# Kernel tuning notes

Measured on AMD Instinct MI355X. Metric: run time of the kernel, lower is better.

Reference implementation:

```python
import jax, jax.numpy as jnp
import numpy as np

B, N, C, H = 8, 1024, 512, 8
EPS = 1e-6


def setup_inputs() -> dict:
    key = jax.random.key(0)
    k0, k1, k2, k3, k4 = jax.random.split(key, 5)
    x = jax.random.normal(k0, (B, N, C), dtype=jnp.float32)
    # nonnegative random-walk visit-frequency mask stand-in
    mask = jax.random.uniform(k1, (N, N), dtype=jnp.float32)
    w_qkv = jax.random.normal(k2, (C, 3 * C), dtype=jnp.float32) * 0.02
    w_out = jax.random.normal(k3, (C, C), dtype=jnp.float32) * 0.02
    b_out = jax.random.normal(k4, (C,), dtype=jnp.float32) * 0.02
    return {"x": x, "mask": mask, "w_qkv": w_qkv, "w_out": w_out, "b_out": b_out}


def reference(x, mask, w_qkv, w_out, b_out):
    b, n, c = x.shape
    d = c // H
    qkv = x @ w_qkv                                   # [B,N,3C]
    q, k, v = jnp.split(qkv, 3, axis=-1)

    def to_heads(t):
        return t.reshape(b, n, H, d).transpose(0, 2, 1, 3)  # [B,H,N,D]

    q, k, v = to_heads(q), to_heads(k), to_heads(v)
    # positive feature map
    q = jax.nn.relu(q) + EPS
    k = jax.nn.relu(k) + EPS
    # graph diffusion: (q^T @ mask)^T == einsum over source node m
    q = q + 0.1 * jnp.einsum('bhmd,mn->bhnd', q, mask)
    k = k + 0.1 * jnp.einsum('bhmd,mn->bhnd', k, mask)
    # linear kernel scores, elementwise-masked
    kernel = jnp.einsum('bhnd,bhmd->bhnm', q, k) * mask   # [B,H,N,N]
    z = 1.0 / (kernel.sum(axis=-1, keepdims=True) + EPS)  # [B,H,N,1]
    out = jnp.einsum('bhnm,bhmd->bhnd', kernel, v) * z    # [B,H,N,D]
    out = out.transpose(0, 2, 1, 3).reshape(b, n, c)      # [B,N,C]
    return out @ w_out + b_out
```

## Files before the change

kernel.cpp:

```cpp
#include <hip/hip_runtime.h>
#include <cstddef>

#define Bsz 8
#define Nn  1024
#define Cc  512
#define Hh  8
#define Dd  64
#define EPSF 1e-6f

typedef __attribute__((ext_vector_type(8))) short short8;
typedef __attribute__((ext_vector_type(4))) float floatx4;

static __device__ __forceinline__ short f2bf(float f) {
    union { float f; unsigned u; } v; v.f = f;
    unsigned r = (v.u + 0x7FFFu + ((v.u >> 16) & 1u)) >> 16;
    return (short)r;
}
static __device__ __forceinline__ float bf2f(short s) {
    union { unsigned u; float f; } v; v.u = ((unsigned)(unsigned short)s) << 16;
    return v.f;
}

#define GLOAD_LDS16(gp, lp)                                              \
    __builtin_amdgcn_global_load_lds(                                    \
        (const __attribute__((address_space(1))) void*)(gp),             \
        (__attribute__((address_space(3))) void*)(lp), 16, 0, 0)

static __device__ __forceinline__
void stage_tile(short* __restrict__ lds, const short* __restrict__ src,
                int ldsrc, int tid, int CHUNKS, int SLOTS) {
    #pragma unroll
    for (int s = tid; s < SLOTS; s += 256) {
        int r = s / CHUNKS, cs = s % CHUNKS;
        int gc = cs ^ (r & 7);
        GLOAD_LDS16(&src[(size_t)r * ldsrc + gc * 8], &lds[s * 8]);
    }
}
static __device__ __forceinline__
short8 fragT(const short* __restrict__ lds, int CHUNKS, int r, int lc) {
    return *(const short8*)&lds[(r * CHUNKS + (lc ^ (r & 7))) * 8];
}

#define FENCE() asm volatile("" ::: "memory")
#define BARRIER_RAW() do { FENCE(); __builtin_amdgcn_s_barrier(); FENCE(); } while (0)
#define WAITVM(N) asm volatile("s_waitcnt vmcnt(" #N ")" ::: "memory")

__global__ __launch_bounds__(256)
void prep_all(const float* __restrict__ x, const float* __restrict__ mask,
              const float* __restrict__ wq, const float* __restrict__ wo,
              short* __restrict__ xb, short* __restrict__ Ad,
              short* __restrict__ wqT, short* __restrict__ woT,
              short* __restrict__ mbf) {
    __shared__ float t[64][65];
    const int tid = threadIdx.x;
    const int bid = blockIdx.x;

    if (bid < 2048) {
        int idx = bid * 256 + tid;
        const float* s = &x[(size_t)idx * 8];
        union { short h[8]; int4 v; } u;
        #pragma unroll
        for (int j = 0; j < 8; j++) u.h[j] = f2bf(s[j]);
        *(int4*)&xb[(size_t)idx * 8] = u.v;
        return;
    }
    if (bid < 2304) {
        int idx = bid - 2048;
        const int n0 = (idx & 15) * 64, m0 = (idx >> 4) * 64;
        #pragma unroll
        for (int i = 0; i < 4; i++) {
            int k = i * 256 + tid;
            int r = k >> 4, c4 = (k & 15) * 4;
            *(float4*)&t[r][c4] = *(const float4*)&mask[(size_t)(m0 + r) * Nn + n0 + c4];
        }
        __syncthreads();
        #pragma unroll
        for (int i = 0; i < 4; i++) {
            int k = i * 256 + tid;
            int rr = k >> 4, c4 = (k & 15) * 4;
            union { short h[4]; int2 v; } u;
            #pragma unroll
            for (int j = 0; j < 4; j++) {
                int mm = c4 + j;
                float v = 0.1f * t[mm][rr] + ((n0 + rr) == (m0 + mm) ? 1.0f : 0.0f);
                u.h[j] = f2bf(v);
            }
            *(int2*)&Ad[(size_t)(n0 + rr) * Nn + m0 + c4] = u.v;
        }
        return;
    }
    if (bid < 2496) {
        int idx = bid - 2304;
        const int n0 = (idx % 24) * 64, k0 = (idx / 24) * 64;
        #pragma unroll
        for (int i = 0; i < 4; i++) {
            int k = i * 256 + tid;
            int r = k >> 4, c4 = (k & 15) * 4;
            *(float4*)&t[r][c4] = *(const float4*)&wq[(size_t)(k0 + r) * 1536 + n0 + c4];
        }
        __syncthreads();
        #pragma unroll
        for (int i = 0; i < 4; i++) {
            int k = i * 256 + tid;
            int rr = k >> 4, c4 = (k & 15) * 4;
            union { short h[4]; int2 v; } u;
            #pragma unroll
            for (int j = 0; j < 4; j++) u.h[j] = f2bf(t[c4 + j][rr]);
            *(int2*)&wqT[(size_t)(n0 + rr) * 512 + k0 + c4] = u.v;
        }
        return;
    }
    if (bid < 2560) {
        int idx = bid - 2496;
        const int n0 = (idx & 7) * 64, k0 = (idx >> 3) * 64;
        #pragma unroll
        for (int i = 0; i < 4; i++) {
            int k = i * 256 + tid;
            int r = k >> 4, c4 = (k & 15) * 4;
            *(float4*)&t[r][c4] = *(const float4*)&wo[(size_t)(k0 + r) * 512 + n0 + c4];
        }
        __syncthreads();
        #pragma unroll
        for (int i = 0; i < 4; i++) {
            int k = i * 256 + tid;
            int rr = k >> 4, c4 = (k & 15) * 4;
            union { short h[4]; int2 v; } u;
            #pragma unroll
            for (int j = 0; j < 4; j++) u.h[j] = f2bf(t[c4 + j][rr]);
            *(int2*)&woT[(size_t)(n0 + rr) * 512 + k0 + c4] = u.v;
        }
        return;
    }
    {
        int idx = (bid - 2560) * 256 + tid;
        const float* s = &mask[(size_t)idx * 8];
        union { short h[8]; int4 v; } u;
        #pragma unroll
        for (int j = 0; j < 8; j++) u.h[j] = f2bf(s[j]);
        *(int4*)&mbf[(size_t)idx * 8] = u.v;
    }
}

static __device__ __forceinline__
void stageA_half(short* __restrict__ buf, const short* __restrict__ gA,
                 int kt, int h, int tid) {
    #pragma unroll
    for (int kk = 0; kk < 2; kk++) {
        int i = tid + kk * 512;
        int run = i >> 9;
        int within = i & 511;
        int r = run * 128 + h * 64 + (within >> 3);
        int c = within & 7;
        int gc = c ^ (r & 7);
        GLOAD_LDS16(gA + (size_t)r * 512 + kt + gc * 8, buf + (r * 8 + c) * 8);
    }
}
static __device__ __forceinline__
void stageB_half(short* __restrict__ buf, const short* __restrict__ gB,
                 int kt, int h, int tid) {
    #pragma unroll
    for (int kk = 0; kk < 2; kk++) {
        int i = tid + kk * 512;
        int run = i >> 8;
        int within = i & 255;
        int r = run * 64 + h * 32 + (within >> 3);
        int c = within & 7;
        int gc = c ^ (r & 7);
        GLOAD_LDS16(gB + (size_t)r * 512 + kt + gc * 8, buf + (r * 8 + c) * 8);
    }
}

template<int MH>
static __device__ __forceinline__
void readA8(const short* __restrict__ bufA, short8 (&aF)[4][2],
            int wr, int l16, int quad) {
    #pragma unroll
    for (int f = 0; f < 4; f++)
        #pragma unroll
        for (int kk = 0; kk < 2; kk++)
            aF[f][kk] = fragT(bufA, 8, wr * 128 + MH * 64 + f * 16 + l16, kk * 4 + quad);
}
template<int NH>
static __device__ __forceinline__
void readB4(const short* __restrict__ bufB, short8 (&bF)[2][2],
            int wc, int l16, int quad) {
    #pragma unroll
    for (int g = 0; g < 2; g++)
        #pragma unroll
        for (int kk = 0; kk < 2; kk++)
            bF[g][kk] = fragT(bufB, 8, wc * 64 + NH * 32 + g * 16 + l16, kk * 4 + quad);
}
template<int MH, int NH>
static __device__ __forceinline__
void mfma16(short8 (&aF)[4][2], short8 (&bF)[2][2], floatx4 (&acc)[8][4]) {
    #pragma unroll
    for (int kk = 0; kk < 2; kk++)
        #pragma unroll
        for (int f = 0; f < 4; f++)
            #pragma unroll
            for (int g = 0; g < 2; g++)
                acc[MH * 4 + f][NH * 2 + g] = __builtin_amdgcn_mfma_f32_16x16x32_bf16(
                    aF[f][kk], bF[g][kk], acc[MH * 4 + f][NH * 2 + g], 0, 0, 0);
}

__global__ __launch_bounds__(512, 2)
void gemm_qkv(const short* __restrict__ xb, const short* __restrict__ wqT,
              short* __restrict__ qT, short* __restrict__ kT,
              short* __restrict__ vT) {
    extern __shared__ short smem[];

    const int tid = threadIdx.x;
    const int lin = blockIdx.x;
    const int wgid = (lin & 7) * 24 + (lin >> 3);
    const int mt = wgid / 6, nt = wgid % 6;
    const int m0 = mt * 256, n0 = nt * 256;

    const int wid = tid >> 6, lane = tid & 63;
    const int quad = lane >> 4, l16 = lane & 15;
    const int wr = wid >> 2, wc = wid & 3;

    const short* Ab = xb  + (size_t)m0 * 512;
    const short* Bb = wqT + (size_t)n0 * 512;

    floatx4 acc[8][4];
    #pragma unroll
    for (int i = 0; i < 8; i++)
        #pragma unroll
        for (int j = 0; j < 4; j++) acc[i][j] = (floatx4){0.f, 0.f, 0.f, 0.f};

    short8 aF[4][2], bF[2][2];

    stageA_half(smem,          Ab, 0, 0, tid);
    stageB_half(smem + 16384,  Bb, 0, 0, tid);
    stageA_half(smem,          Ab, 0, 1, tid);
    stageB_half(smem + 16384,  Bb, 0, 1, tid);
    WAITVM(4); BARRIER_RAW();

    for (int j = 0; j < 8; ++j) {
        const short* cA = smem + (j & 1) * 32768;
        const short* cB = cA + 16384;
        short* nA = smem + ((j + 1) & 1) * 32768;
        short* nB = nA + 16384;
        const int kn = ((j + 1) & 7) * 64;

        readA8<0>(cA, aF, wr, l16, quad);
        readB4<0>(cB, bF, wc, l16, quad);
        stageA_half(nA, Ab, kn, 0, tid);
        stageB_half(nB, Bb, kn, 0, tid);
        BARRIER_RAW();
        __builtin_amdgcn_s_setprio(1);
        mfma16<0, 0>(aF, bF, acc);
        __builtin_amdgcn_s_setprio(0);
        WAITVM(4); BARRIER_RAW();

        readA8<1>(cA, aF, wr, l16, quad);
        stageA_half(nA, Ab, kn, 1, tid);
        stageB_half(nB, Bb, kn, 1, tid);
        BARRIER_RAW();
        __builtin_amdgcn_s_setprio(1);
        mfma16<1, 0>(aF, bF, acc);
        __builtin_amdgcn_s_setprio(0);
        BARRIER_RAW();

        readB4<1>(cB, bF, wc, l16, quad);
        BARRIER_RAW();
        __builtin_amdgcn_s_setprio(1);
        mfma16<1, 1>(aF, bF, acc);
        __builtin_amdgcn_s_setprio(0);
        BARRIER_RAW();

        readA8<0>(cA, aF, wr, l16, quad);
        BARRIER_RAW();
        __builtin_amdgcn_s_setprio(1);
        mfma16<0, 1>(aF, bF, acc);
        __builtin_amdgcn_s_setprio(0);
        WAITVM(4); BARRIER_RAW();
    }

    WAITVM(0); BARRIER_RAW();

    short* T = smem + wid * 8192;
    const int doRelu = (n0 < 1024);
    #pragma unroll
    for (int mf = 0; mf < 8; mf++)
        #pragma unroll
        for (int nf = 0; nf < 4; nf++)
            #pragma unroll
            for (int rr = 0; rr < 4; rr++) {
                float v = acc[mf][nf][rr];
                if (doRelu) v = fmaxf(v, 0.0f) + EPSF;
                int row = nf * 16 + l16;
                int col = mf * 16 + quad * 4 + rr;
                T[row * 128 + (col ^ ((row & 15) << 3))] = f2bf(v);
            }
    const int gm0 = m0 + wr * 128;
    const int b = gm0 >> 10, m_in0 = gm0 & 1023;
    #pragma unroll
    for (int g = 0; g < 4; g++) {
        int row = (lane >> 2) + g * 16;
        int gn = n0 + wc * 64 + row;
        int part = gn >> 9, ci = gn & 511;
        short* base = (part == 0) ? qT : (part == 1) ? kT : vT;
        short* dst = base + ((size_t)b * 512 + ci) * 1024 + m_in0;
        #pragma unroll
        for (int cc = 0; cc < 4; cc++) {
            int cs = ((lane & 3) + cc * 4) * 8;
            *(int4*)&dst[cs] = *(const int4*)&T[row * 128 + (cs ^ ((row & 15) << 3))];
        }
    }
}

static __device__ __forceinline__
void dstageA_half(short* __restrict__ buf, const short* __restrict__ gA,
                  int kt, int h, int tid) {
    #pragma unroll
    for (int kk = 0; kk < 2; kk++) {
        int i = tid + kk * 512;
        int rl = i >> 3;
        int c  = i & 7;
        int r  = (rl >> 5) * 64 + h * 32 + (rl & 31);
        int gc = c ^ (r & 7);
        GLOAD_LDS16(gA + (size_t)r * 1024 + kt + gc * 8, buf + (r * 8 + c) * 8);
    }
}
static __device__ __forceinline__
void dstageB_half(short* __restrict__ buf, const short* __restrict__ gB,
                  int kt, int h, int tid) {
    int rl = tid >> 3;
    int c  = tid & 7;
    int r  = (rl >> 5) * 64 + h * 32 + (rl & 31);
    int gc = c ^ (r & 7);
    GLOAD_LDS16(gB + (size_t)r * 1024 + kt + gc * 8, buf + (r * 8 + c) * 8);
}
template<int MH>
static __device__ __forceinline__
void dreadA(const short* __restrict__ bufA, short8 (&aF)[2][2],
            int wr, int l16, int quad) {
    #pragma unroll
    for (int f = 0; f < 2; f++)
        #pragma unroll
        for (int kk = 0; kk < 2; kk++)
            aF[f][kk] = fragT(bufA, 8, wr * 64 + MH * 32 + f * 16 + l16, kk * 4 + quad);
}
template<int NH>
static __device__ __forceinline__
void dreadB(const short* __restrict__ bufB, short8 (&bF)[2][2],
            int wc, int l16, int quad) {
    #pragma unroll
    for (int g = 0; g < 2; g++)
        #pragma unroll
        for (int kk = 0; kk < 2; kk++)
            bF[g][kk] = fragT(bufB, 8, wc * 64 + NH * 32 + g * 16 + l16, kk * 4 + quad);
}
template<int MH, int NH>
static __device__ __forceinline__
void dmfma8(short8 (&aF)[2][2], short8 (&bF)[2][2], floatx4 (&acc)[4][4]) {
    #pragma unroll
    for (int kk = 0; kk < 2; kk++)
        #pragma unroll
        for (int f = 0; f < 2; f++)
            #pragma unroll
            for (int g = 0; g < 2; g++)
                acc[MH * 2 + f][NH * 2 + g] = __builtin_amdgcn_mfma_f32_16x16x32_bf16(
                    aF[f][kk], bF[g][kk], acc[MH * 2 + f][NH * 2 + g], 0, 0, 0);
}

__global__ __launch_bounds__(512, 2)
void gemm_diff8(const short* __restrict__ Ad, const short* __restrict__ qT,
                const short* __restrict__ kT, short* __restrict__ qd,
                short* __restrict__ kd) {
    extern __shared__ short smem[];

    const int tid = threadIdx.x;
    const int lin = blockIdx.x;
    const int wgid = (lin & 7) * 32 + (lin >> 3);
    const int mt = wgid >> 6, ct = wgid & 63;
    const int m0 = mt * 256;
    const int seg = ct >> 2, cb = (ct & 3) * 128;
    const int b = seg >> 1, part = seg & 1;

    const short* Bb = ((part ? kT : qT) + (size_t)b * 512 * 1024) + (size_t)cb * 1024;
    short* outb = (part ? kd : qd) + (size_t)b * 1024 * 512;
    const short* Abase = Ad + (size_t)m0 * 1024;

    const int wid = tid >> 6, lane = tid & 63;
    const int quad = lane >> 4, l16 = lane & 15;
    const int wr = wid >> 1, wc = wid & 1;

    floatx4 acc[4][4];
    #pragma unroll
    for (int i = 0; i < 4; i++)
        #pragma unroll
        for (int j = 0; j < 4; j++) acc[i][j] = (floatx4){0.f, 0.f, 0.f, 0.f};

    short8 aF[2][2], bF[2][2];

    dstageA_half(smem,          Abase, 0, 0, tid);
    dstageB_half(smem + 16384,  Bb,    0, 0, tid);
    dstageA_half(smem,          Abase, 0, 1, tid);
    dstageB_half(smem + 16384,  Bb,    0, 1, tid);
    WAITVM(3); BARRIER_RAW();

    for (int j = 0; j < 16; ++j) {
        const short* cA = smem + (j & 1) * 24576;
        const short* cB = cA + 16384;
        short* nA = smem + ((j + 1) & 1) * 24576;
        short* nB = nA + 16384;
        const int kn = ((j + 1) & 15) * 64;

        dreadA<0>(cA, aF, wr, l16, quad);
        dreadB<0>(cB, bF, wc, l16, quad);
        dstageA_half(nA, Abase, kn, 0, tid);
        dstageB_half(nB, Bb,    kn, 0, tid);
        BARRIER_RAW();
        __builtin_amdgcn_s_setprio(1);
        dmfma8<0, 0>(aF, bF, acc);
        __builtin_amdgcn_s_setprio(0);
        WAITVM(3); BARRIER_RAW();

        dreadA<1>(cA, aF, wr, l16, quad);
        dstageA_half(nA, Abase, kn, 1, tid);
        dstageB_half(nB, Bb,    kn, 1, tid);
        BARRIER_RAW();
        __builtin_amdgcn_s_setprio(1);
        dmfma8<1, 0>(aF, bF, acc);
        __builtin_amdgcn_s_setprio(0);
        BARRIER_RAW();

        dreadB<1>(cB, bF, wc, l16, quad);
        BARRIER_RAW();
        __builtin_amdgcn_s_setprio(1);
        dmfma8<1, 1>(aF, bF, acc);
        __builtin_amdgcn_s_setprio(0);
        BARRIER_RAW();

        dreadA<0>(cA, aF, wr, l16, quad);
        BARRIER_RAW();
        __builtin_amdgcn_s_setprio(1);
        dmfma8<0, 1>(aF, bF, acc);
        __builtin_amdgcn_s_setprio(0);
        WAITVM(3); BARRIER_RAW();
    }
    WAITVM(0);

    #pragma unroll
    for (int fr = 0; fr < 4; fr++)
        #pragma unroll
        for (int rr = 0; rr < 4; rr++) {
            int n = m0 + wr * 64 + fr * 16 + quad * 4 + rr;
            #pragma unroll
            for (int fc = 0; fc < 4; fc++) {
                int c = cb + wc * 64 + fc * 16 + l16;
                outb[(size_t)n * 512 + c] = f2bf(acc[fr][fc][rr]);
            }
        }
}

__global__ __launch_bounds__(256)
void attn_mfma(const short* __restrict__ qd, const short* __restrict__ kd,
               const short* __restrict__ vTg, const short* __restrict__ mbf,
               short* __restrict__ abf) {
    __shared__ short qs[8192];
    __shared__ short ks[4096];
    __shared__ short vt[4096];
    __shared__ short ss[8192];
    __shared__ short ms[8192];

    const int tid = threadIdx.x;
    const int bh = blockIdx.x;
    const int b = bh >> 3, h = bh & 7;
    const int n0 = blockIdx.y * 128;

    const int wave = tid >> 6, lane = tid & 63;
    const int quad = lane >> 4, l16 = lane & 15;

    const short* Qb = qd + ((size_t)b * Nn + n0) * Cc + h * Dd;
    const short* Kb = kd + (size_t)b * Nn * Cc + h * Dd;
    const short* Vb = vTg + ((size_t)b * Cc + h * Dd) * Nn;
    const short* Mb = mbf + (size_t)n0 * Nn;

    stage_tile(qs, Qb, Cc, tid, 8, 1024);
    __syncthreads();
    short8 aT[2][2];
    #pragma unroll
    for (int t = 0; t < 2; t++) {
        aT[t][0] = fragT(qs, 8, wave * 32 + t * 16 + l16, quad);
        aT[t][1] = fragT(qs, 8, wave * 32 + t * 16 + l16, 4 + quad);
    }

    float dreg[2] = {0.f, 0.f};
    floatx4 nacc[2][4];
    #pragma unroll
    for (int t = 0; t < 2; t++)
        #pragma unroll
        for (int i = 0; i < 4; i++) nacc[t][i] = (floatx4){0.f, 0.f, 0.f, 0.f};

    const int ssrow[2] = { wave * 32 + l16, wave * 32 + 16 + l16 };

    for (int m0 = 0; m0 < Nn; m0 += 64) {
        __syncthreads();
        stage_tile(ks, Kb + (size_t)m0 * Cc, Cc, tid, 8, 512);
        stage_tile(vt, Vb + m0, Nn, tid, 8, 512);
        stage_tile(ms, Mb + m0, Nn, tid, 8, 1024);
        __syncthreads();

        #pragma unroll
        for (int mt = 0; mt < 4; mt++) {
            const short8 k0f = fragT(ks, 8, mt * 16 + l16, quad);
            const short8 k1f = fragT(ks, 8, mt * 16 + l16, 4 + quad);
            #pragma unroll
            for (int t = 0; t < 2; t++) {
                floatx4 s = (floatx4){0.f, 0.f, 0.f, 0.f};
                s = __builtin_amdgcn_mfma_f32_16x16x32_bf16(k0f, aT[t][0], s, 0, 0, 0);
                s = __builtin_amdgcn_mfma_f32_16x16x32_bf16(k1f, aT[t][1], s, 0, 0, 0);
                const int row = ssrow[t];
                const int c = mt * 16 + quad * 4;
                const int off = (row * 8 + ((c >> 3) ^ (row & 7))) * 8 + (c & 7);
                union { short h[4]; int2 v; } mk;
                mk.v = *(const int2*)&ms[off];
                float sv0 = s[0] * bf2f(mk.h[0]);
                float sv1 = s[1] * bf2f(mk.h[1]);
                float sv2 = s[2] * bf2f(mk.h[2]);
                float sv3 = s[3] * bf2f(mk.h[3]);
                dreg[t] += (sv0 + sv1) + (sv2 + sv3);
                union { short h[4]; int2 v; } pk;
                pk.h[0] = f2bf(sv0); pk.h[1] = f2bf(sv1);
                pk.h[2] = f2bf(sv2); pk.h[3] = f2bf(sv3);
                *(int2*)&ss[off] = pk.v;
            }
        }

        short8 p[2][2];
        #pragma unroll
        for (int t = 0; t < 2; t++) {
            p[t][0] = fragT(ss, 8, wave * 32 + t * 16 + l16, quad);
            p[t][1] = fragT(ss, 8, wave * 32 + t * 16 + l16, 4 + quad);
        }
        #pragma unroll
        for (int dt = 0; dt < 4; dt++) {
            const short8 v0 = fragT(vt, 8, dt * 16 + l16, quad);
            const short8 v1 = fragT(vt, 8, dt * 16 + l16, 4 + quad);
            #pragma unroll
            for (int t = 0; t < 2; t++) {
                nacc[t][dt] = __builtin_amdgcn_mfma_f32_16x16x32_bf16(p[t][0], v0, nacc[t][dt], 0, 0, 0);
                nacc[t][dt] = __builtin_amdgcn_mfma_f32_16x16x32_bf16(p[t][1], v1, nacc[t][dt], 0, 0, 0);
            }
        }
    }

    #pragma unroll
    for (int t = 0; t < 2; t++) {
        dreg[t] += __shfl_xor(dreg[t], 16, 64);
        dreg[t] += __shfl_xor(dreg[t], 32, 64);
    }

    #pragma unroll
    for (int t = 0; t < 2; t++)
        #pragma unroll
        for (int r = 0; r < 4; r++) {
            int nloc = quad * 4 + r;
            float den = __shfl(dreg[t], nloc, 64);
            int n = n0 + wave * 32 + t * 16 + nloc;
            float zr = 1.0f / (den + EPSF);
            #pragma unroll
            for (int dt = 0; dt < 4; dt++) {
                size_t o = ((size_t)b * Nn + n) * Cc + h * Dd + dt * 16 + l16;
                abf[o] = f2bf(nacc[t][dt][r] * zr);
            }
        }
}

__global__ __launch_bounds__(256)
void gemm_out(const short* __restrict__ abf, const short* __restrict__ woT,
              const float* __restrict__ bias, float* __restrict__ out) {
    __shared__ short smem[12288];
    short* As = smem;
    short* Bs = smem + 4096;

    const int tid = threadIdx.x;
    const int m0 = blockIdx.y * 64;
    const int n0 = blockIdx.x * 128;
    const int wave = tid >> 6, lane = tid & 63;
    const int quad = lane >> 4, l16 = lane & 15;
    const int wm = (wave >> 1) * 32, wn = (wave & 1) * 64;

    floatx4 acc[2][4];
    #pragma unroll
    for (int i = 0; i < 2; i++)
        #pragma unroll
        for (int j = 0; j < 4; j++) acc[i][j] = (floatx4){0.f, 0.f, 0.f, 0.f};

    const short* Ab = abf + (size_t)m0 * 512;
    const short* Bb = woT + (size_t)n0 * 512;

    for (int k0 = 0; k0 < 512; k0 += 64) {
        __syncthreads();
        stage_tile(As, Ab + k0, 512, tid, 8, 512);
        stage_tile(Bs, Bb + k0, 512, tid, 8, 1024);
        __syncthreads();
        #pragma unroll
        for (int kh = 0; kh < 2; kh++) {
            short8 a[2], b[4];
            #pragma unroll
            for (int i = 0; i < 2; i++)
                a[i] = fragT(As, 8, wm + i * 16 + l16, kh * 4 + quad);
            #pragma unroll
            for (int i = 0; i < 4; i++)
                b[i] = fragT(Bs, 8, wn + i * 16 + l16, kh * 4 + quad);
            #pragma unroll
            for (int mi = 0; mi < 2; mi++)
                #pragma unroll
                for (int ni = 0; ni < 4; ni++)
                    acc[mi][ni] = __builtin_amdgcn_mfma_f32_16x16x32_bf16(
                        a[mi], b[ni], acc[mi][ni], 0, 0, 0);
        }
    }

    #pragma unroll
    for (int mi = 0; mi < 2; mi++)
        #pragma unroll
        for (int r = 0; r < 4; r++) {
            int m = m0 + wm + mi * 16 + quad * 4 + r;
            #pragma unroll
            for (int ni = 0; ni < 4; ni++) {
                int n = n0 + wn + ni * 16 + l16;
                out[(size_t)m * 512 + n] = acc[mi][ni][r] + bias[n];
            }
        }
}

extern "C" void kernel_launch(void* const* d_in, const int* in_sizes, int n_in,
                              void* d_out, int out_size, void* d_ws, size_t ws_size,
                              hipStream_t stream) {
    const float* x     = (const float*)d_in[0];
    const float* mask  = (const float*)d_in[1];
    const float* w_qkv = (const float*)d_in[2];
    const float* w_out = (const float*)d_in[3];
    const float* b_out = (const float*)d_in[4];
    float* out = (float*)d_out;

    char* p = (char*)d_ws;
    short* xb  = (short*)p; p += 8388608;
    short* wqT = (short*)p; p += 1572864;
    short* Ad  = (short*)p; p += 2097152;
    short* woT = (short*)p; p += 524288;
    short* mbf = (short*)p; p += 2097152;
    short* qT  = (short*)p; p += 8388608;
    short* kT  = (short*)p; p += 8388608;
    short* vT  = (short*)p; p += 8388608;
    short* qd  = (short*)p; p += 8388608;
    short* kd  = (short*)p; p += 8388608;
    short* abf = (short*)p; p += 8388608;

    static int attr_set = 0;
    if (!attr_set) {
        hipFuncSetAttribute(reinterpret_cast<const void*>(gemm_qkv),
                            hipFuncAttributeMaxDynamicSharedMemorySize, 131072);
        hipFuncSetAttribute(reinterpret_cast<const void*>(gemm_diff8),
                            hipFuncAttributeMaxDynamicSharedMemorySize, 98304);
        attr_set = 1;
    }

    dim3 blk(256);

    prep_all  <<<3072, blk, 0, stream>>>(x, mask, w_qkv, w_out,
                                         xb, Ad, wqT, woT, mbf);
    gemm_qkv  <<<dim3(192), dim3(512), 131072, stream>>>(xb, wqT, qT, kT, vT);
    gemm_diff8<<<dim3(256), dim3(512), 98304, stream>>>(Ad, qT, kT, qd, kd);
    attn_mfma <<<dim3(64, 8),  blk, 0, stream>>>(qd, kd, vT, mbf, abf);
    gemm_out  <<<dim3(4, 128), blk, 0, stream>>>(abf, woT, b_out, out);
}
```

Baseline: 166.2 us.

## Double-buffer K/V tiles in attention kernel and load mask directly to registers

Restructures the attention kernel's main loop into a two-stage ping-pong pipeline. The next K/V tile is staged into a second LDS buffer while the current tile is computed. Mask values are loaded straight from global memory into registers instead of going through LDS, and the Q staging buffer is reused for the score scratch once Q fragments are in registers. It also packs bf16 conversion with v_cvt_pk_bf16_f32 and raises wave priority around the PV MFMAs. The goal is to hide global load latency and cut barriers and LDS traffic, at the cost of more registers and reliance on raw barrier and waitcnt ordering for correctness.

```diff
diff --git a/kernel.cpp b/kernel.cpp
--- a/kernel.cpp
+++ b/kernel.cpp
@@ -456,15 +456,63 @@
         }
 }
 
+static __device__ __forceinline__
+void attn_tile(const short* __restrict__ ks, const short* __restrict__ vt,
+               short* __restrict__ ss, const int2 (&M)[2][4],
+               const short8 (&aT)[2][2], float (&dreg)[2],
+               floatx4 (&nacc)[2][4], int wave, int quad, int l16) {
+    const int ssrow[2] = { wave * 32 + l16, wave * 32 + 16 + l16 };
+    #pragma unroll
+    for (int mt = 0; mt < 4; mt++) {
+        const short8 k0f = fragT(ks, 8, mt * 16 + l16, quad);
+        const short8 k1f = fragT(ks, 8, mt * 16 + l16, 4 + quad);
+        #pragma unroll
+        for (int t = 0; t < 2; t++) {
+            floatx4 s = (floatx4){0.f, 0.f, 0.f, 0.f};
+            s = __builtin_amdgcn_mfma_f32_16x16x32_bf16(k0f, aT[t][0], s, 0, 0, 0);
+            s = __builtin_amdgcn_mfma_f32_16x16x32_bf16(k1f, aT[t][1], s, 0, 0, 0);
+            const int row = ssrow[t];
+            const int c = mt * 16 + quad * 4;
+            const int off = (row * 8 + ((c >> 3) ^ (row & 7))) * 8 + (c & 7);
+            union { short hh[4]; int2 v; } mk; mk.v = M[t][mt];
+            float sv0 = s[0] * bf2f(mk.hh[0]);
+            float sv1 = s[1] * bf2f(mk.hh[1]);
+            float sv2 = s[2] * bf2f(mk.hh[2]);
+            float sv3 = s[3] * bf2f(mk.hh[3]);
+            dreg[t] += (sv0 + sv1) + (sv2 + sv3);
+            int lo, hi;
+            asm("v_cvt_pk_bf16_f32 %0, %1, %2" : "=v"(lo) : "v"(sv0), "v"(sv1));
+            asm("v_cvt_pk_bf16_f32 %0, %1, %2" : "=v"(hi) : "v"(sv2), "v"(sv3));
+            int2 pv; pv.x = lo; pv.y = hi;
+            *(int2*)&ss[off] = pv;
+        }
+    }
+    short8 p[2][2];
+    #pragma unroll
+    for (int t = 0; t < 2; t++) {
+        p[t][0] = fragT(ss, 8, wave * 32 + t * 16 + l16, quad);
+        p[t][1] = fragT(ss, 8, wave * 32 + t * 16 + l16, 4 + quad);
+    }
+    __builtin_amdgcn_s_setprio(1);
+    #pragma unroll
+    for (int dt = 0; dt < 4; dt++) {
+        const short8 v0 = fragT(vt, 8, dt * 16 + l16, quad);
+        const short8 v1 = fragT(vt, 8, dt * 16 + l16, 4 + quad);
+        #pragma unroll
+        for (int t = 0; t < 2; t++) {
+            nacc[t][dt] = __builtin_amdgcn_mfma_f32_16x16x32_bf16(p[t][0], v0, nacc[t][dt], 0, 0, 0);
+            nacc[t][dt] = __builtin_amdgcn_mfma_f32_16x16x32_bf16(p[t][1], v1, nacc[t][dt], 0, 0, 0);
+        }
+    }
+    __builtin_amdgcn_s_setprio(0);
+}
+
 __global__ __launch_bounds__(256)
 void attn_mfma(const short* __restrict__ qd, const short* __restrict__ kd,
                const short* __restrict__ vTg, const short* __restrict__ mbf,
                short* __restrict__ abf) {
-    __shared__ short qs[8192];
-    __shared__ short ks[4096];
-    __shared__ short vt[4096];
-    __shared__ short ss[8192];
-    __shared__ short ms[8192];
+    __shared__ short qss[8192];
+    __shared__ short kv[2][8192];
 
     const int tid = threadIdx.x;
     const int bh = blockIdx.x;
@@ -477,15 +525,24 @@
     const short* Qb = qd + ((size_t)b * Nn + n0) * Cc + h * Dd;
     const short* Kb = kd + (size_t)b * Nn * Cc + h * Dd;
     const short* Vb = vTg + ((size_t)b * Cc + h * Dd) * Nn;
-    const short* Mb = mbf + (size_t)n0 * Nn;
-
-    stage_tile(qs, Qb, Cc, tid, 8, 1024);
-    __syncthreads();
+    const short* baseM = mbf + (size_t)(n0 + wave * 32 + l16) * Nn + quad * 4;
+
+    stage_tile(qss, Qb, Cc, tid, 8, 1024);
+    stage_tile(kv[0],        Kb, Cc, tid, 8, 512);
+    stage_tile(kv[0] + 4096, Vb, Nn, tid, 8, 512);
+    int2 Ma[2][4], Mb2[2][4];
+    #pragma unroll
+    for (int t = 0; t < 2; t++)
+        #pragma unroll
+        for (int mt = 0; mt < 4; mt++)
+            Ma[t][mt] = *(const int2*)(baseM + t * 16 * Nn + mt * 16);
+    WAITVM(0); BARRIER_RAW();
+
     short8 aT[2][2];
     #pragma unroll
     for (int t = 0; t < 2; t++) {
-        aT[t][0] = fragT(qs, 8, wave * 32 + t * 16 + l16, quad);
-        aT[t][1] = fragT(qs, 8, wave * 32 + t * 16 + l16, 4 + quad);
+        aT[t][0] = fragT(qss, 8, wave * 32 + t * 16 + l16, quad);
+        aT[t][1] = fragT(qss, 8, wave * 32 + t * 16 + l16, 4 + quad);
     }
 
     float dreg[2] = {0.f, 0.f};
@@ -495,57 +552,29 @@
         #pragma unroll
         for (int i = 0; i < 4; i++) nacc[t][i] = (floatx4){0.f, 0.f, 0.f, 0.f};
 
-    const int ssrow[2] = { wave * 32 + l16, wave * 32 + 16 + l16 };
-
-    for (int m0 = 0; m0 < Nn; m0 += 64) {
-        __syncthreads();
-        stage_tile(ks, Kb + (size_t)m0 * Cc, Cc, tid, 8, 512);
-        stage_tile(vt, Vb + m0, Nn, tid, 8, 512);
-        stage_tile(ms, Mb + m0, Nn, tid, 8, 1024);
-        __syncthreads();
-
-        #pragma unroll
-        for (int mt = 0; mt < 4; mt++) {
-            const short8 k0f = fragT(ks, 8, mt * 16 + l16, quad);
-            const short8 k1f = fragT(ks, 8, mt * 16 + l16, 4 + quad);
-            #pragma unroll
-            for (int t = 0; t < 2; t++) {
-                floatx4 s = (floatx4){0.f, 0.f, 0.f, 0.f};
-                s = __builtin_amdgcn_mfma_f32_16x16x32_bf16(k0f, aT[t][0], s, 0, 0, 0);
-                s = __builtin_amdgcn_mfma_f32_16x16x32_bf16(k1f, aT[t][1], s, 0, 0, 0);
-                const int row = ssrow[t];
-                const int c = mt * 16 + quad * 4;
-                const int off = (row * 8 + ((c >> 3) ^ (row & 7))) * 8 + (c & 7);
-                union { short h[4]; int2 v; } mk;
-                mk.v = *(const int2*)&ms[off];
-                float sv0 = s[0] * bf2f(mk.h[0]);
-                float sv1 = s[1] * bf2f(mk.h[1]);
-                float sv2 = s[2] * bf2f(mk.h[2]);
-                float sv3 = s[3] * bf2f(mk.h[3]);
-                dreg[t] += (sv0 + sv1) + (sv2 + sv3);
-                union { short h[4]; int2 v; } pk;
-                pk.h[0] = f2bf(sv0); pk.h[1] = f2bf(sv1);
-                pk.h[2] = f2bf(sv2); pk.h[3] = f2bf(sv3);
-                *(int2*)&ss[off] = pk.v;
-            }
-        }
-
-        short8 p[2][2];
-        #pragma unroll
-        for (int t = 0; t < 2; t++) {
-            p[t][0] = fragT(ss, 8, wave * 32 + t * 16 + l16, quad);
-            p[t][1] = fragT(ss, 8, wave * 32 + t * 16 + l16, 4 + quad);
-        }
-        #pragma unroll
-        for (int dt = 0; dt < 4; dt++) {
-            const short8 v0 = fragT(vt, 8, dt * 16 + l16, quad);
-            const short8 v1 = fragT(vt, 8, dt * 16 + l16, 4 + quad);
-            #pragma unroll
-            for (int t = 0; t < 2; t++) {
-                nacc[t][dt] = __builtin_amdgcn_mfma_f32_16x16x32_bf16(p[t][0], v0, nacc[t][dt], 0, 0, 0);
-                nacc[t][dt] = __builtin_amdgcn_mfma_f32_16x16x32_bf16(p[t][1], v1, nacc[t][dt], 0, 0, 0);
-            }
-        }
+    for (int jo = 0; jo < 8; jo++) {
+        const int j0 = jo * 2;
+        stage_tile(kv[1],        Kb + (size_t)(j0 + 1) * 64 * Cc, Cc, tid, 8, 512);
+        stage_tile(kv[1] + 4096, Vb + (j0 + 1) * 64,              Nn, tid, 8, 512);
+        #pragma unroll
+        for (int t = 0; t < 2; t++)
+            #pragma unroll
+            for (int mt = 0; mt < 4; mt++)
+                Mb2[t][mt] = *(const int2*)(baseM + t * 16 * Nn + (j0 + 1) * 64 + mt * 16);
+        attn_tile(kv[0], kv[0] + 4096, qss, Ma, aT, dreg, nacc, wave, quad, l16);
+        WAITVM(0); BARRIER_RAW();
+
+        if (jo < 7) {
+            stage_tile(kv[0],        Kb + (size_t)(j0 + 2) * 64 * Cc, Cc, tid, 8, 512);
+            stage_tile(kv[0] + 4096, Vb + (j0 + 2) * 64,              Nn, tid, 8, 512);
+            #pragma unroll
+            for (int t = 0; t < 2; t++)
+                #pragma unroll
+                for (int mt = 0; mt < 4; mt++)
+                    Ma[t][mt] = *(const int2*)(baseM + t * 16 * Nn + (j0 + 2) * 64 + mt * 16);
+        }
+        attn_tile(kv[1], kv[1] + 4096, qss, Mb2, aT, dreg, nacc, wave, quad, l16);
+        WAITVM(0); BARRIER_RAW();
     }
 
     #pragma unroll
```

Measured after the change: 174.4 us. +5.0%, slower.

## Use 32x32x16 MFMA in attention and keep scores in registers via lane shuffles

Applied to the files above, without the earlier changes.

Rewrites the attention inner loop around 32x32x16 bf16 MFMA instead of 16x16x32. The masked score tile goes straight from the S accumulator layout into the A-operand layout of the PV MFMA through packed bf16 conversions and cross-half lane shuffles, which removes the shared-memory round trip through ss. It also raises wave priority around the PV MFMAs. The aims are fewer LDS writes and reads, less shared memory per block, and better MFMA efficiency. The cost is more shuffle and select instructions and a fragile register layout mapping.

```diff
diff --git a/kernel.cpp b/kernel.cpp
--- a/kernel.cpp
+++ b/kernel.cpp
@@ -10,6 +10,7 @@
 
 typedef __attribute__((ext_vector_type(8))) short short8;
 typedef __attribute__((ext_vector_type(4))) float floatx4;
+typedef __attribute__((ext_vector_type(16))) float floatx16;
 
 static __device__ __forceinline__ short f2bf(float f) {
     union { float f; unsigned u; } v; v.f = f;
@@ -463,7 +464,6 @@
     __shared__ short qs[8192];
     __shared__ short ks[4096];
     __shared__ short vt[4096];
-    __shared__ short ss[8192];
     __shared__ short ms[8192];
 
     const int tid = threadIdx.x;
@@ -472,7 +472,7 @@
     const int n0 = blockIdx.y * 128;
 
     const int wave = tid >> 6, lane = tid & 63;
-    const int quad = lane >> 4, l16 = lane & 15;
+    const int l32 = lane & 31, hi = lane >> 5;
 
     const short* Qb = qd + ((size_t)b * Nn + n0) * Cc + h * Dd;
     const short* Kb = kd + (size_t)b * Nn * Cc + h * Dd;
@@ -481,21 +481,15 @@
 
     stage_tile(qs, Qb, Cc, tid, 8, 1024);
     __syncthreads();
-    short8 aT[2][2];
-    #pragma unroll
-    for (int t = 0; t < 2; t++) {
-        aT[t][0] = fragT(qs, 8, wave * 32 + t * 16 + l16, quad);
-        aT[t][1] = fragT(qs, 8, wave * 32 + t * 16 + l16, 4 + quad);
-    }
-
-    float dreg[2] = {0.f, 0.f};
-    floatx4 nacc[2][4];
-    #pragma unroll
-    for (int t = 0; t < 2; t++)
-        #pragma unroll
-        for (int i = 0; i < 4; i++) nacc[t][i] = (floatx4){0.f, 0.f, 0.f, 0.f};
-
-    const int ssrow[2] = { wave * 32 + l16, wave * 32 + 16 + l16 };
+    short8 qf[4];
+    #pragma unroll
+    for (int j = 0; j < 4; j++)
+        qf[j] = fragT(qs, 8, wave * 32 + l32, 2 * j + hi);
+
+    float dreg = 0.f;
+    floatx16 nacc0, nacc1;
+    #pragma unroll
+    for (int i = 0; i < 16; i++) { nacc0[i] = 0.f; nacc1[i] = 0.f; }
 
     for (int m0 = 0; m0 < Nn; m0 += 64) {
         __syncthreads();
@@ -505,68 +499,83 @@
         __syncthreads();
 
         #pragma unroll
-        for (int mt = 0; mt < 4; mt++) {
-            const short8 k0f = fragT(ks, 8, mt * 16 + l16, quad);
-            const short8 k1f = fragT(ks, 8, mt * 16 + l16, 4 + quad);
-            #pragma unroll
-            for (int t = 0; t < 2; t++) {
-                floatx4 s = (floatx4){0.f, 0.f, 0.f, 0.f};
-                s = __builtin_amdgcn_mfma_f32_16x16x32_bf16(k0f, aT[t][0], s, 0, 0, 0);
-                s = __builtin_amdgcn_mfma_f32_16x16x32_bf16(k1f, aT[t][1], s, 0, 0, 0);
-                const int row = ssrow[t];
-                const int c = mt * 16 + quad * 4;
-                const int off = (row * 8 + ((c >> 3) ^ (row & 7))) * 8 + (c & 7);
-                union { short h[4]; int2 v; } mk;
+        for (int msub = 0; msub < 2; msub++) {
+            floatx16 S;
+            #pragma unroll
+            for (int i = 0; i < 16; i++) S[i] = 0.f;
+            #pragma unroll
+            for (int j = 0; j < 4; j++) {
+                const short8 kf = fragT(ks, 8, msub * 32 + l32, 2 * j + hi);
+                S = __builtin_amdgcn_mfma_f32_32x32x16_bf16(kf, qf[j], S, 0, 0, 0);
+            }
+            const int mrow = wave * 32 + l32;
+            float sv[16];
+            int w[8];
+            #pragma unroll
+            for (int g = 0; g < 4; g++) {
+                const int c = msub * 4 + g;
+                const int off = (mrow * 8 + (c ^ (mrow & 7))) * 8 + hi * 4;
+                union { short hh[4]; int2 v; } mk;
                 mk.v = *(const int2*)&ms[off];
-                float sv0 = s[0] * bf2f(mk.h[0]);
-                float sv1 = s[1] * bf2f(mk.h[1]);
-                float sv2 = s[2] * bf2f(mk.h[2]);
-                float sv3 = s[3] * bf2f(mk.h[3]);
-                dreg[t] += (sv0 + sv1) + (sv2 + sv3);
-                union { short h[4]; int2 v; } pk;
-                pk.h[0] = f2bf(sv0); pk.h[1] = f2bf(sv1);
-                pk.h[2] = f2bf(sv2); pk.h[3] = f2bf(sv3);
-                *(int2*)&ss[off] = pk.v;
+                #pragma unroll
+                for (int ri = 0; ri < 4; ri++) {
+                    float s = S[4 * g + ri] * bf2f(mk.hh[ri]);
+                    sv[4 * g + ri] = s;
+                    dreg += s;
+                }
+                int wl, wh;
+                asm("v_cvt_pk_bf16_f32 %0, %1, %2"
+                    : "=v"(wl) : "v"(sv[4 * g]), "v"(sv[4 * g + 1]));
+                asm("v_cvt_pk_bf16_f32 %0, %1, %2"
+                    : "=v"(wh) : "v"(sv[4 * g + 2]), "v"(sv[4 * g + 3]));
+                w[2 * g] = wl; w[2 * g + 1] = wh;
             }
-        }
-
-        short8 p[2][2];
-        #pragma unroll
-        for (int t = 0; t < 2; t++) {
-            p[t][0] = fragT(ss, 8, wave * 32 + t * 16 + l16, quad);
-            p[t][1] = fragT(ss, 8, wave * 32 + t * 16 + l16, 4 + quad);
-        }
-        #pragma unroll
-        for (int dt = 0; dt < 4; dt++) {
-            const short8 v0 = fragT(vt, 8, dt * 16 + l16, quad);
-            const short8 v1 = fragT(vt, 8, dt * 16 + l16, 4 + quad);
-            #pragma unroll
-            for (int t = 0; t < 2; t++) {
-                nacc[t][dt] = __builtin_amdgcn_mfma_f32_16x16x32_bf16(p[t][0], v0, nacc[t][dt], 0, 0, 0);
-                nacc[t][dt] = __builtin_amdgcn_mfma_f32_16x16x32_bf16(p[t][1], v1, nacc[t][dt], 0, 0, 0);
+            int sx[8];
+            #pragma unroll
+            for (int i = 0; i < 8; i++) sx[i] = __shfl_xor(w[i], 32, 64);
+            union { int wi[4]; short8 v; } pa0, pa1;
+            pa0.wi[0] = hi ? sx[2] : w[0];
+            pa0.wi[1] = hi ? sx[3] : w[1];
+            pa0.wi[2] = hi ? w[2]  : sx[0];
+            pa0.wi[3] = hi ? w[3]  : sx[1];
+            pa1.wi[0] = hi ? sx[6] : w[4];
+            pa1.wi[1] = hi ? sx[7] : w[5];
+            pa1.wi[2] = hi ? w[6]  : sx[4];
+            pa1.wi[3] = hi ? w[7]  : sx[5];
+            __builtin_amdgcn_s_setprio(1);
+            {
+                const short8 v00 = fragT(vt, 8, 0 * 32 + l32, msub * 4 + 0 + hi);
+                const short8 v01 = fragT(vt, 8, 0 * 32 + l32, msub * 4 + 2 + hi);
+                nacc0 = __builtin_amdgcn_mfma_f32_32x32x16_bf16(pa0.v, v00, nacc0, 0, 0, 0);
+                nacc0 = __builtin_amdgcn_mfma_f32_32x32x16_bf16(pa1.v, v01, nacc0, 0, 0, 0);
+                const short8 v10 = fragT(vt, 8, 1 * 32 + l32, msub * 4 + 0 + hi);
+                const short8 v11 = fragT(vt, 8, 1 * 32 + l32, msub * 4 + 2 + hi);
+                nacc1 = __builtin_amdgcn_mfma_f32_32x32x16_bf16(pa0.v, v10, nacc1, 0, 0, 0);
+                nacc1 = __builtin_amdgcn_mfma_f32_32x32x16_bf16(pa1.v, v11, nacc1, 0, 0, 0);
             }
-        }
-    }
-
-    #pragma unroll
-    for (int t = 0; t < 2; t++) {
-        dreg[t] += __shfl_xor(dreg[t], 16, 64);
-        dreg[t] += __shfl_xor(dreg[t], 32, 64);
-    }
-
-    #pragma unroll
-    for (int t = 0; t < 2; t++)
-        #pragma unroll
-        for (int r = 0; r < 4; r++) {
-            int nloc = quad * 4 + r;
-            float den = __shfl(dreg[t], nloc, 64);
-            int n = n0 + wave * 32 + t * 16 + nloc;
-            float zr = 1.0f / (den + EPSF);
-            #pragma unroll
-            for (int dt = 0; dt < 4; dt++) {
-                size_t o = ((size_t)b * Nn + n) * Cc + h * Dd + dt * 16 + l16;
-                abf[o] = f2bf(nacc[t][dt][r] * zr);
-            }
+            __builtin_amdgcn_s_setprio(0);
+        }
+    }
+
+    dreg += __shfl_xor(dreg, 32, 64);
+
+    float den16[16];
+    #pragma unroll
+    for (int g = 0; g < 4; g++)
+        #pragma unroll
+        for (int ri = 0; ri < 4; ri++)
+            den16[4 * g + ri] = __shfl(dreg, 8 * g + 4 * hi + ri, 64);
+
+    #pragma unroll
+    for (int g = 0; g < 4; g++)
+        #pragma unroll
+        for (int ri = 0; ri < 4; ri++) {
+            const int nl = 8 * g + 4 * hi + ri;
+            const int n = n0 + wave * 32 + nl;
+            const float zr = 1.0f / (den16[4 * g + ri] + EPSF);
+            size_t o = ((size_t)b * Nn + n) * Cc + h * Dd + l32;
+            abf[o]      = f2bf(nacc0[4 * g + ri] * zr);
+            abf[o + 32] = f2bf(nacc1[4 * g + ri] * zr);
         }
 }
 
```

Result: no change. 169.0 us (+1.7%).
